# Performance work log

Hardware: AMD Instinct MI355X
Metric: run time of the kernel (lower is better)

Reference implementation:

```python
import jax, jax.numpy as jnp
import numpy as np

N_NODES = 50000
N_EDGES = 640000
N_REL = 8
D_IN = 128
D_HID = 128
D_OUT = 64


def setup_inputs() -> dict:
    key = jax.random.key(0)
    ks = jax.random.split(key, 10)
    x = jax.random.normal(ks[0], (N_NODES, D_IN), dtype=jnp.float32)
    edge_src = jax.random.randint(ks[1], (N_EDGES,), 0, N_NODES, dtype=jnp.int32)
    edge_dst = jax.random.randint(ks[2], (N_EDGES,), 0, N_NODES, dtype=jnp.int32)
    edge_type = jax.random.randint(ks[3], (N_EDGES,), 0, N_REL, dtype=jnp.int32)
    # Glorot-ish scaling for stability
    W1 = jax.random.normal(ks[4], (N_REL, D_IN, D_HID), dtype=jnp.float32) / np.sqrt(D_IN)
    root1 = jax.random.normal(ks[5], (D_IN, D_HID), dtype=jnp.float32) / np.sqrt(D_IN)
    b1 = jnp.zeros((D_HID,), dtype=jnp.float32)
    W2 = jax.random.normal(ks[6], (N_REL, D_HID, D_OUT), dtype=jnp.float32) / np.sqrt(D_HID)
    root2 = jax.random.normal(ks[7], (D_HID, D_OUT), dtype=jnp.float32) / np.sqrt(D_HID)
    b2 = jnp.zeros((D_OUT,), dtype=jnp.float32)
    return {"x": x, "edge_src": edge_src, "edge_dst": edge_dst, "edge_type": edge_type,
            "W1": W1, "root1": root1, "b1": b1, "W2": W2, "root2": root2, "b2": b2}


def rgcn_conv(x, edge_src, edge_dst, edge_type, W, W_root, b):
    """RGCNConv with default per-relation mean aggregation + root weight + bias."""
    N = x.shape[0]
    R, _, O = W.shape
    # Transform all nodes under all relation weights once: [N, R, O]
    xW = jnp.einsum('nd,rdo->nro', x, W)
    # Gather per-edge relation-specific messages: [E, O]
    msg = xW[edge_src, edge_type]
    # Segment per (dst, relation) for mean aggregation
    seg = edge_dst.astype(jnp.int32) * R + edge_type.astype(jnp.int32)
    cnt = jax.ops.segment_sum(jnp.ones_like(edge_type, dtype=x.dtype), seg, num_segments=N * R)
    agg = jax.ops.segment_sum(msg, seg, num_segments=N * R)  # [N*R, O]
    agg = agg / jnp.maximum(cnt, 1.0)[:, None]
    rel_sum = agg.reshape(N, R, O).sum(axis=1)  # [N, O]
    return rel_sum + x @ W_root + b


def reference(x, edge_src, edge_dst, edge_type, W1, root1, b1, W2, root2, b2):
    h = rgcn_conv(x, edge_src, edge_dst, edge_type, W1, root1, b1)
    h = rgcn_conv(h, edge_src, edge_dst, edge_type, W2, root2, b2)
    return jax.nn.sigmoid(h)
```

## Files before the change

### kernel.cpp

```cpp
#include <hip/hip_runtime.h>
#include <math.h>

#define NN 50000
#define NE 640000
#define NR 8
#define KT 1152
#define KA 1024
#define SCAN_N (NN * NR)
#define SCAN_CH 2048
#define SCAN_NB ((SCAN_N + SCAN_CH - 1) / SCAN_CH)

typedef __attribute__((ext_vector_type(8))) _Float16 half8;
typedef __attribute__((ext_vector_type(8))) short short8;
typedef __attribute__((ext_vector_type(4))) float f32x4;
typedef const void __attribute__((address_space(1))) gvoid_t;
typedef void __attribute__((address_space(3))) svoid_t;

__device__ __forceinline__ unsigned short f2h(float f) {
    _Float16 h = (_Float16)f;
    return __builtin_bit_cast(unsigned short, h);
}
__device__ __forceinline__ float h2f(unsigned short u) {
    return (float)__builtin_bit_cast(_Float16, u);
}

__global__ __launch_bounds__(256) void count_kernel(const int* __restrict__ dst,
                                                    const int* __restrict__ typ,
                                                    int* __restrict__ cnt, int E) {
    int e = blockIdx.x * 256 + threadIdx.x;
    if (e < E) atomicAdd(&cnt[dst[e] * NR + typ[e]], 1);
}

__global__ __launch_bounds__(256) void inv_kernel(const int* __restrict__ cnt,
                                                  float* __restrict__ inv, int n) {
    int i = blockIdx.x * 256 + threadIdx.x;
    if (i < n) {
        int c = cnt[i];
        inv[i] = 1.0f / (float)(c > 1 ? c : 1);
    }
}

__global__ __launch_bounds__(256) void scan1_kernel(const int* __restrict__ cnt,
                                                    int* __restrict__ loc,
                                                    int* __restrict__ bsum) {
    __shared__ int s[256];
    const int t = threadIdx.x;
    const int base = blockIdx.x * SCAN_CH + t * 8;
    int v[8];
    int sum = 0;
#pragma unroll
    for (int j = 0; j < 8; ++j) {
        int idx = base + j;
        v[j] = (idx < SCAN_N) ? cnt[idx] : 0;
        sum += v[j];
    }
    s[t] = sum;
    __syncthreads();
    for (int off = 1; off < 256; off <<= 1) {
        int u = (t >= off) ? s[t - off] : 0;
        __syncthreads();
        s[t] += u;
        __syncthreads();
    }
    int run = (t == 0) ? 0 : s[t - 1];
#pragma unroll
    for (int j = 0; j < 8; ++j) {
        int idx = base + j;
        if (idx < SCAN_N) loc[idx] = run;
        run += v[j];
    }
    if (t == 255) bsum[blockIdx.x] = s[255];
}

__global__ __launch_bounds__(256) void scan2_kernel(const int* __restrict__ bsum,
                                                    int* __restrict__ boff, int nb) {
    __shared__ int s[256];
    const int t = threadIdx.x;
    s[t] = (t < nb) ? bsum[t] : 0;
    __syncthreads();
    for (int off = 1; off < 256; off <<= 1) {
        int u = (t >= off) ? s[t - off] : 0;
        __syncthreads();
        s[t] += u;
        __syncthreads();
    }
    if (t < nb) boff[t] = (t == 0) ? 0 : s[t - 1];
    if (t == nb - 1) boff[nb] = s[t];
}

__global__ __launch_bounds__(256) void scan3_kernel(int* __restrict__ rowptr,
                                                    int* __restrict__ start,
                                                    const int* __restrict__ boff, int nb) {
    const int b = blockIdx.x, t = threadIdx.x;
    const int add = boff[b];
#pragma unroll
    for (int j = 0; j < 8; ++j) {
        int idx = b * SCAN_CH + t * 8 + j;
        if (idx < SCAN_N) {
            int v = rowptr[idx] + add;
            rowptr[idx] = v;
            start[idx] = v;
        }
    }
    if (b == 0 && t == 0) rowptr[SCAN_N] = boff[nb];
}

__global__ __launch_bounds__(256) void fill_kernel(const int* __restrict__ src,
                                                   const int* __restrict__ dst,
                                                   const int* __restrict__ typ,
                                                   int* __restrict__ start,
                                                   int* __restrict__ srcrel, int E) {
    int e = blockIdx.x * 256 + threadIdx.x;
    if (e >= E) return;
    int r = typ[e];
    int pos = atomicAdd(&start[dst[e] * NR + r], 1);
    srcrel[pos] = src[e] | (r << 20);
}

__global__ __launch_bounds__(256) void cvt_kernel(const float* __restrict__ x,
                                                  unsigned short* __restrict__ xh, int n4) {
    int i = blockIdx.x * 256 + threadIdx.x;
    if (i >= n4) return;
    float4 v = ((const float4*)x)[i];
    uint2 u;
    u.x = (unsigned)f2h(v.x) | ((unsigned)f2h(v.y) << 16);
    u.y = (unsigned)f2h(v.z) | ((unsigned)f2h(v.w) << 16);
    ((uint2*)xh)[i] = u;
}

__global__ __launch_bounds__(256) void pack_b_kernel(const float* __restrict__ W,
                                                     const float* __restrict__ root,
                                                     unsigned short* __restrict__ Bt, int N) {
    int i = blockIdx.x * 256 + threadIdx.x;
    if (i >= N * KT) return;
    int k = i % KT, n = i / KT;
    float v = (k < 1024) ? W[(size_t)k * N + n] : root[(size_t)(k - 1024) * N + n];
    Bt[(size_t)n * KT + k] = f2h(v);
}

__global__ __launch_bounds__(256) void agg_kernel(const int* __restrict__ rp,
                                                  const int* __restrict__ srcrel,
                                                  const float* __restrict__ inv,
                                                  const unsigned short* __restrict__ X,
                                                  unsigned short* __restrict__ A) {
    __shared__ float acc[4][NR][128];
    const int slot = threadIdx.x >> 6, lane = threadIdx.x & 63;
    const int w = blockIdx.x * 4 + slot;
    if (w >= NN) return;

#pragma unroll
    for (int r = 0; r < NR; ++r)
        *(float2*)&acc[slot][r][lane * 2] = make_float2(0.f, 0.f);

    const unsigned int* X2 = (const unsigned int*)X;
    const int beg = rp[w * NR], end = rp[w * NR + NR];

    int i = beg;
    const int n2 = beg + ((end - beg) & ~1);
    for (; i < n2; i += 2) {
        int p0 = srcrel[i], p1 = srcrel[i + 1];
        unsigned h0 = X2[(size_t)(p0 & 0xFFFFF) * 64 + lane];
        unsigned h1 = X2[(size_t)(p1 & 0xFFFFF) * 64 + lane];
        {
            float2* a = (float2*)&acc[slot][((unsigned)p0) >> 20][lane * 2];
            float2 c = *a;
            c.x += h2f((unsigned short)(h0 & 0xFFFFu));
            c.y += h2f((unsigned short)(h0 >> 16));
            *a = c;
        }
        {
            float2* a = (float2*)&acc[slot][((unsigned)p1) >> 20][lane * 2];
            float2 c = *a;
            c.x += h2f((unsigned short)(h1 & 0xFFFFu));
            c.y += h2f((unsigned short)(h1 >> 16));
            *a = c;
        }
    }
    if (i < end) {
        int p0 = srcrel[i];
        unsigned h0 = X2[(size_t)(p0 & 0xFFFFF) * 64 + lane];
        float2* a = (float2*)&acc[slot][((unsigned)p0) >> 20][lane * 2];
        float2 c = *a;
        c.x += h2f((unsigned short)(h0 & 0xFFFFu));
        c.y += h2f((unsigned short)(h0 >> 16));
        *a = c;
    }

    unsigned int* Arow = (unsigned int*)(A + (size_t)w * KA);
#pragma unroll
    for (int r = 0; r < NR; ++r) {
        float sc = inv[w * NR + r];
        float2 v = *(float2*)&acc[slot][r][lane * 2];
        Arow[r * 64 + lane] = (unsigned)f2h(v.x * sc) | ((unsigned)f2h(v.y * sc) << 16);
    }
}

template <int NT, bool FINAL>
__global__ __launch_bounds__(256) void gemm_f16(const unsigned short* __restrict__ A,
                                                const unsigned short* __restrict__ Aroot,
                                                const unsigned short* __restrict__ Bt,
                                                const float* __restrict__ bias,
                                                void* __restrict__ Cout) {
    __shared__ __align__(16) unsigned short As[64 * 64];
    __shared__ __align__(16) unsigned short Bs[NT * 64];
    const int t = threadIdx.x;
    const int w = t >> 6, lane = t & 63;
    const int q = lane >> 4, m = lane & 15;
    const int wr = w >> 1, wc = w & 1;
    const int bm = blockIdx.x * 64;
    constexpr int WNB = NT / 32;

    f32x4 acc[2][WNB];
#pragma unroll
    for (int mb = 0; mb < 2; ++mb)
#pragma unroll
        for (int nb = 0; nb < WNB; ++nb) acc[mb][nb] = (f32x4)0.f;

    const int srow = lane >> 3, schk = lane & 7;

    for (int k0 = 0; k0 < KT; k0 += 64) {
#pragma unroll
        for (int ii = 0; ii < 2; ++ii) {
            int i = w * 2 + ii;
            int grow = bm + i * 8 + srow;
            if (grow >= NN) grow = NN - 1;
            const unsigned short* g =
                (k0 < KA) ? A + (size_t)grow * KA + k0 + schk * 8
                          : Aroot + (size_t)grow * 128 + (k0 - KA) + schk * 8;
            __builtin_amdgcn_global_load_lds((gvoid_t*)g, (svoid_t*)(As + i * 512), 16, 0, 0);
        }
#pragma unroll
        for (int ii = 0; ii < NT / 32; ++ii) {
            int i = w * (NT / 32) + ii;
            int row = i * 8 + srow;
            const unsigned short* g = Bt + (size_t)row * KT + k0 + schk * 8;
            __builtin_amdgcn_global_load_lds((gvoid_t*)g, (svoid_t*)(Bs + i * 512), 16, 0, 0);
        }
        __syncthreads();
#pragma unroll
        for (int s = 0; s < 2; ++s) {
            half8 af[2], bf[WNB];
#pragma unroll
            for (int mb = 0; mb < 2; ++mb)
                af[mb] = __builtin_bit_cast(half8,
                    *(const short8*)(As + (wr * 32 + mb * 16 + m) * 64 + s * 32 + q * 8));
#pragma unroll
            for (int nb = 0; nb < WNB; ++nb)
                bf[nb] = __builtin_bit_cast(half8,
                    *(const short8*)(Bs + (wc * (NT / 2) + nb * 16 + m) * 64 + s * 32 + q * 8));
#pragma unroll
            for (int mb = 0; mb < 2; ++mb)
#pragma unroll
                for (int nb = 0; nb < WNB; ++nb)
                    acc[mb][nb] = __builtin_amdgcn_mfma_f32_16x16x32_f16(af[mb], bf[nb],
                                                                         acc[mb][nb], 0, 0, 0);
        }
        __syncthreads();
    }

#pragma unroll
    for (int mb = 0; mb < 2; ++mb)
#pragma unroll
        for (int nb = 0; nb < WNB; ++nb) {
            int col = wc * (NT / 2) + nb * 16 + m;
            float bv = bias[col];
#pragma unroll
            for (int j = 0; j < 4; ++j) {
                int grow = bm + wr * 32 + mb * 16 + q * 4 + j;
                if (grow < NN) {
                    float v = acc[mb][nb][j] + bv;
                    if (FINAL)
                        ((float*)Cout)[(size_t)grow * NT + col] = 1.f / (1.f + __expf(-v));
                    else
                        ((unsigned short*)Cout)[(size_t)grow * NT + col] = f2h(v);
                }
            }
        }
}

extern "C" void kernel_launch(void* const* d_in, const int* in_sizes, int n_in,
                              void* d_out, int out_size, void* d_ws, size_t ws_size,
                              hipStream_t stream) {
    const float* x     = (const float*)d_in[0];
    const int*   esrc  = (const int*)d_in[1];
    const int*   edst  = (const int*)d_in[2];
    const int*   etyp  = (const int*)d_in[3];
    const float* W1    = (const float*)d_in[4];
    const float* root1 = (const float*)d_in[5];
    const float* b1    = (const float*)d_in[6];
    const float* W2    = (const float*)d_in[7];
    const float* root2 = (const float*)d_in[8];
    const float* b2    = (const float*)d_in[9];
    float* out = (float*)d_out;

    char* ws = (char*)d_ws;
    unsigned short* Bt1    = (unsigned short*)ws; ws += (size_t)128 * KT * 2;
    unsigned short* Bt2    = (unsigned short*)ws; ws += (size_t)64 * KT * 2;
    int*            cnt    = (int*)ws;            ws += (size_t)SCAN_N * 4;
    float*          inv    = (float*)ws;          ws += (size_t)SCAN_N * 4;
    int*            rp     = (int*)ws;            ws += (size_t)(SCAN_N + 64) * 4;
    int*            start  = (int*)ws;            ws += (size_t)SCAN_N * 4;
    int*            bsum   = (int*)ws;            ws += (size_t)256 * 4;
    int*            boff   = (int*)ws;            ws += (size_t)257 * 4;
    int*            srcrel = (int*)ws;            ws += (size_t)NE * 4;
    unsigned short* xh     = (unsigned short*)ws; ws += (size_t)NN * 128 * 2;
    unsigned short* h1b    = (unsigned short*)ws; ws += (size_t)NN * 128 * 2;
    unsigned short* Abig   = (unsigned short*)ws;

    hipMemsetAsync(cnt, 0, (size_t)SCAN_N * 4, stream);
    count_kernel<<<(NE + 255) / 256, 256, 0, stream>>>(edst, etyp, cnt, NE);
    inv_kernel<<<(SCAN_N + 255) / 256, 256, 0, stream>>>(cnt, inv, SCAN_N);
    scan1_kernel<<<SCAN_NB, 256, 0, stream>>>(cnt, rp, bsum);
    scan2_kernel<<<1, 256, 0, stream>>>(bsum, boff, SCAN_NB);
    scan3_kernel<<<SCAN_NB, 256, 0, stream>>>(rp, start, boff, SCAN_NB);
    fill_kernel<<<(NE + 255) / 256, 256, 0, stream>>>(esrc, edst, etyp, start, srcrel, NE);

    cvt_kernel<<<(NN * 32 + 255) / 256, 256, 0, stream>>>(x, xh, NN * 32);
    pack_b_kernel<<<(128 * KT + 255) / 256, 256, 0, stream>>>(W1, root1, Bt1, 128);
    pack_b_kernel<<<(64 * KT + 255) / 256, 256, 0, stream>>>(W2, root2, Bt2, 64);

    const int agrid = (NN + 3) / 4;
    const int ggrid = (NN + 63) / 64;

    agg_kernel<<<agrid, 256, 0, stream>>>(rp, srcrel, inv, xh, Abig);
    gemm_f16<128, false><<<ggrid, 256, 0, stream>>>(Abig, xh, Bt1, b1, h1b);

    agg_kernel<<<agrid, 256, 0, stream>>>(rp, srcrel, inv, h1b, Abig);
    gemm_f16<64, true><<<ggrid, 256, 0, stream>>>(Abig, h1b, Bt2, b2, out);
}
```

Measured before the change: 348.9 us.

## Reorder RGCN to transform-then-gather and fuse mean, root and bias into aggregation

Instead of aggregating raw features per relation into a wide A matrix and running a K=1152 GEMM, each layer first computes x times all relation and root weights into an N×(9·O) fp16 buffer. An aggregation kernel then gathers relation-specific rows per edge, scales by inverse counts, and adds root and bias (plus sigmoid at the end). This removes the shared-memory per-relation accumulators and shrinks layer-2 gather width, at the cost of writing a large intermediate transform buffer.

```diff
diff --git a/kernel.cpp b/kernel.cpp
--- a/kernel.cpp
+++ b/kernel.cpp
@@ -4,8 +4,6 @@
 #define NN 50000
 #define NE 640000
 #define NR 8
-#define KT 1152
-#define KA 1024
 #define SCAN_N (NN * NR)
 #define SCAN_CH 2048
 #define SCAN_NB ((SCAN_N + SCAN_CH - 1) / SCAN_CH)
@@ -130,128 +128,70 @@
 
 __global__ __launch_bounds__(256) void pack_b_kernel(const float* __restrict__ W,
                                                      const float* __restrict__ root,
-                                                     unsigned short* __restrict__ Bt, int N) {
+                                                     unsigned short* __restrict__ Bt, int O) {
     int i = blockIdx.x * 256 + threadIdx.x;
-    if (i >= N * KT) return;
-    int k = i % KT, n = i / KT;
-    float v = (k < 1024) ? W[(size_t)k * N + n] : root[(size_t)(k - 1024) * N + n];
-    Bt[(size_t)n * KT + k] = f2h(v);
-}
-
-__global__ __launch_bounds__(256) void agg_kernel(const int* __restrict__ rp,
-                                                  const int* __restrict__ srcrel,
-                                                  const float* __restrict__ inv,
-                                                  const unsigned short* __restrict__ X,
-                                                  unsigned short* __restrict__ A) {
-    __shared__ float acc[4][NR][128];
-    const int slot = threadIdx.x >> 6, lane = threadIdx.x & 63;
-    const int w = blockIdx.x * 4 + slot;
-    if (w >= NN) return;
-
-#pragma unroll
-    for (int r = 0; r < NR; ++r)
-        *(float2*)&acc[slot][r][lane * 2] = make_float2(0.f, 0.f);
-
-    const unsigned int* X2 = (const unsigned int*)X;
-    const int beg = rp[w * NR], end = rp[w * NR + NR];
-
-    int i = beg;
-    const int n2 = beg + ((end - beg) & ~1);
-    for (; i < n2; i += 2) {
-        int p0 = srcrel[i], p1 = srcrel[i + 1];
-        unsigned h0 = X2[(size_t)(p0 & 0xFFFFF) * 64 + lane];
-        unsigned h1 = X2[(size_t)(p1 & 0xFFFFF) * 64 + lane];
-        {
-            float2* a = (float2*)&acc[slot][((unsigned)p0) >> 20][lane * 2];
-            float2 c = *a;
-            c.x += h2f((unsigned short)(h0 & 0xFFFFu));
-            c.y += h2f((unsigned short)(h0 >> 16));
-            *a = c;
-        }
-        {
-            float2* a = (float2*)&acc[slot][((unsigned)p1) >> 20][lane * 2];
-            float2 c = *a;
-            c.x += h2f((unsigned short)(h1 & 0xFFFFu));
-            c.y += h2f((unsigned short)(h1 >> 16));
-            *a = c;
-        }
-    }
-    if (i < end) {
-        int p0 = srcrel[i];
-        unsigned h0 = X2[(size_t)(p0 & 0xFFFFF) * 64 + lane];
-        float2* a = (float2*)&acc[slot][((unsigned)p0) >> 20][lane * 2];
-        float2 c = *a;
-        c.x += h2f((unsigned short)(h0 & 0xFFFFu));
-        c.y += h2f((unsigned short)(h0 >> 16));
-        *a = c;
-    }
-
-    unsigned int* Arow = (unsigned int*)(A + (size_t)w * KA);
-#pragma unroll
-    for (int r = 0; r < NR; ++r) {
-        float sc = inv[w * NR + r];
-        float2 v = *(float2*)&acc[slot][r][lane * 2];
-        Arow[r * 64 + lane] = (unsigned)f2h(v.x * sc) | ((unsigned)f2h(v.y * sc) << 16);
-    }
-}
-
-template <int NT, bool FINAL>
-__global__ __launch_bounds__(256) void gemm_f16(const unsigned short* __restrict__ A,
-                                                const unsigned short* __restrict__ Aroot,
-                                                const unsigned short* __restrict__ Bt,
-                                                const float* __restrict__ bias,
-                                                void* __restrict__ Cout) {
+    int NTOT = 9 * O;
+    if (i >= NTOT * 128) return;
+    int k = i & 127, n = i >> 7;
+    float v = (n < 8 * O) ? W[(size_t)(n / O) * 128 * O + (size_t)k * O + (n % O)]
+                          : root[(size_t)k * O + (n - 8 * O)];
+    Bt[(size_t)n * 128 + k] = f2h(v);
+}
+
+template <int LDC>
+__global__ __launch_bounds__(256) void gemm_xw(const unsigned short* __restrict__ A,
+                                               const unsigned short* __restrict__ Bt,
+                                               unsigned short* __restrict__ C) {
     __shared__ __align__(16) unsigned short As[64 * 64];
-    __shared__ __align__(16) unsigned short Bs[NT * 64];
+    __shared__ __align__(16) unsigned short Bs[64 * 64];
     const int t = threadIdx.x;
     const int w = t >> 6, lane = t & 63;
     const int q = lane >> 4, m = lane & 15;
     const int wr = w >> 1, wc = w & 1;
-    const int bm = blockIdx.x * 64;
-    constexpr int WNB = NT / 32;
-
-    f32x4 acc[2][WNB];
+    const int bm = blockIdx.y * 64;
+    const int bn = blockIdx.x * 64;
+
+    f32x4 acc[2][2];
 #pragma unroll
     for (int mb = 0; mb < 2; ++mb)
 #pragma unroll
-        for (int nb = 0; nb < WNB; ++nb) acc[mb][nb] = (f32x4)0.f;
+        for (int nb = 0; nb < 2; ++nb) acc[mb][nb] = (f32x4)0.f;
 
     const int srow = lane >> 3, schk = lane & 7;
 
-    for (int k0 = 0; k0 < KT; k0 += 64) {
+#pragma unroll
+    for (int kc = 0; kc < 2; ++kc) {
+        const int k0 = kc * 64;
 #pragma unroll
         for (int ii = 0; ii < 2; ++ii) {
             int i = w * 2 + ii;
             int grow = bm + i * 8 + srow;
             if (grow >= NN) grow = NN - 1;
-            const unsigned short* g =
-                (k0 < KA) ? A + (size_t)grow * KA + k0 + schk * 8
-                          : Aroot + (size_t)grow * 128 + (k0 - KA) + schk * 8;
+            const unsigned short* g = A + (size_t)grow * 128 + k0 + schk * 8;
             __builtin_amdgcn_global_load_lds((gvoid_t*)g, (svoid_t*)(As + i * 512), 16, 0, 0);
         }
 #pragma unroll
-        for (int ii = 0; ii < NT / 32; ++ii) {
-            int i = w * (NT / 32) + ii;
-            int row = i * 8 + srow;
-            const unsigned short* g = Bt + (size_t)row * KT + k0 + schk * 8;
+        for (int ii = 0; ii < 2; ++ii) {
+            int i = w * 2 + ii;
+            const unsigned short* g = Bt + (size_t)(bn + i * 8 + srow) * 128 + k0 + schk * 8;
             __builtin_amdgcn_global_load_lds((gvoid_t*)g, (svoid_t*)(Bs + i * 512), 16, 0, 0);
         }
         __syncthreads();
 #pragma unroll
         for (int s = 0; s < 2; ++s) {
-            half8 af[2], bf[WNB];
+            half8 af[2], bf[2];
 #pragma unroll
             for (int mb = 0; mb < 2; ++mb)
                 af[mb] = __builtin_bit_cast(half8,
                     *(const short8*)(As + (wr * 32 + mb * 16 + m) * 64 + s * 32 + q * 8));
 #pragma unroll
-            for (int nb = 0; nb < WNB; ++nb)
+            for (int nb = 0; nb < 2; ++nb)
                 bf[nb] = __builtin_bit_cast(half8,
-                    *(const short8*)(Bs + (wc * (NT / 2) + nb * 16 + m) * 64 + s * 32 + q * 8));
+                    *(const short8*)(Bs + (wc * 32 + nb * 16 + m) * 64 + s * 32 + q * 8));
 #pragma unroll
             for (int mb = 0; mb < 2; ++mb)
 #pragma unroll
-                for (int nb = 0; nb < WNB; ++nb)
+                for (int nb = 0; nb < 2; ++nb)
                     acc[mb][nb] = __builtin_amdgcn_mfma_f32_16x16x32_f16(af[mb], bf[nb],
                                                                          acc[mb][nb], 0, 0, 0);
         }
@@ -261,21 +201,92 @@
 #pragma unroll
     for (int mb = 0; mb < 2; ++mb)
 #pragma unroll
-        for (int nb = 0; nb < WNB; ++nb) {
-            int col = wc * (NT / 2) + nb * 16 + m;
-            float bv = bias[col];
+        for (int nb = 0; nb < 2; ++nb) {
+            int col = bn + wc * 32 + nb * 16 + m;
 #pragma unroll
             for (int j = 0; j < 4; ++j) {
                 int grow = bm + wr * 32 + mb * 16 + q * 4 + j;
-                if (grow < NN) {
-                    float v = acc[mb][nb][j] + bv;
-                    if (FINAL)
-                        ((float*)Cout)[(size_t)grow * NT + col] = 1.f / (1.f + __expf(-v));
-                    else
-                        ((unsigned short*)Cout)[(size_t)grow * NT + col] = f2h(v);
-                }
+                if (grow < NN)
+                    C[(size_t)grow * LDC + col] = f2h(acc[mb][nb][j]);
             }
         }
+}
+
+template <int O, bool FINAL>
+__global__ __launch_bounds__(256) void agg_kernel(const int* __restrict__ rp,
+                                                  const int* __restrict__ srcrel,
+                                                  const float* __restrict__ inv,
+                                                  const unsigned short* __restrict__ XW,
+                                                  const float* __restrict__ bias,
+                                                  void* __restrict__ Hout) {
+    __shared__ float sinv[4][8];
+    const int slot = threadIdx.x >> 6, lane = threadIdx.x & 63;
+    const int w = blockIdx.x * 4 + slot;
+    if (w >= NN) return;
+    if (lane < 8) sinv[slot][lane] = inv[w * NR + lane];
+
+    const int beg = rp[w * NR], end = rp[w * NR + NR];
+    constexpr int LDC2 = 9 * O / 2;
+
+    if (O == 128) {
+        const unsigned int* X2 = (const unsigned int*)XW;
+        float2 acc = make_float2(0.f, 0.f);
+        int i = beg;
+        for (; i + 3 < end; i += 4) {
+            int p0 = srcrel[i], p1 = srcrel[i + 1], p2 = srcrel[i + 2], p3 = srcrel[i + 3];
+            unsigned g0 = X2[(size_t)(p0 & 0xFFFFF) * LDC2 + (((unsigned)p0) >> 20) * 64 + lane];
+            unsigned g1 = X2[(size_t)(p1 & 0xFFFFF) * LDC2 + (((unsigned)p1) >> 20) * 64 + lane];
+            unsigned g2 = X2[(size_t)(p2 & 0xFFFFF) * LDC2 + (((unsigned)p2) >> 20) * 64 + lane];
+            unsigned g3 = X2[(size_t)(p3 & 0xFFFFF) * LDC2 + (((unsigned)p3) >> 20) * 64 + lane];
+            float s0 = sinv[slot][((unsigned)p0) >> 20];
+            float s1 = sinv[slot][((unsigned)p1) >> 20];
+            float s2 = sinv[slot][((unsigned)p2) >> 20];
+            float s3 = sinv[slot][((unsigned)p3) >> 20];
+            acc.x += h2f((unsigned short)(g0 & 0xFFFFu)) * s0;
+            acc.y += h2f((unsigned short)(g0 >> 16)) * s0;
+            acc.x += h2f((unsigned short)(g1 & 0xFFFFu)) * s1;
+            acc.y += h2f((unsigned short)(g1 >> 16)) * s1;
+            acc.x += h2f((unsigned short)(g2 & 0xFFFFu)) * s2;
+            acc.y += h2f((unsigned short)(g2 >> 16)) * s2;
+            acc.x += h2f((unsigned short)(g3 & 0xFFFFu)) * s3;
+            acc.y += h2f((unsigned short)(g3 >> 16)) * s3;
+        }
+        for (; i < end; ++i) {
+            int p0 = srcrel[i];
+            unsigned g0 = X2[(size_t)(p0 & 0xFFFFF) * LDC2 + (((unsigned)p0) >> 20) * 64 + lane];
+            float s0 = sinv[slot][((unsigned)p0) >> 20];
+            acc.x += h2f((unsigned short)(g0 & 0xFFFFu)) * s0;
+            acc.y += h2f((unsigned short)(g0 >> 16)) * s0;
+        }
+        unsigned rt = X2[(size_t)w * LDC2 + 512 + lane];
+        float2 bv = ((const float2*)bias)[lane];
+        float vx = acc.x + h2f((unsigned short)(rt & 0xFFFFu)) + bv.x;
+        float vy = acc.y + h2f((unsigned short)(rt >> 16)) + bv.y;
+        ((unsigned int*)Hout)[(size_t)w * 64 + lane] =
+            (unsigned)f2h(vx) | ((unsigned)f2h(vy) << 16);
+    } else {
+        constexpr int LDC = 9 * O;
+        float acc = 0.f;
+        int i = beg;
+        for (; i + 3 < end; i += 4) {
+            int p0 = srcrel[i], p1 = srcrel[i + 1], p2 = srcrel[i + 2], p3 = srcrel[i + 3];
+            unsigned short g0 = XW[(size_t)(p0 & 0xFFFFF) * LDC + (((unsigned)p0) >> 20) * 64 + lane];
+            unsigned short g1 = XW[(size_t)(p1 & 0xFFFFF) * LDC + (((unsigned)p1) >> 20) * 64 + lane];
+            unsigned short g2 = XW[(size_t)(p2 & 0xFFFFF) * LDC + (((unsigned)p2) >> 20) * 64 + lane];
+            unsigned short g3 = XW[(size_t)(p3 & 0xFFFFF) * LDC + (((unsigned)p3) >> 20) * 64 + lane];
+            acc += h2f(g0) * sinv[slot][((unsigned)p0) >> 20];
+            acc += h2f(g1) * sinv[slot][((unsigned)p1) >> 20];
+            acc += h2f(g2) * sinv[slot][((unsigned)p2) >> 20];
+            acc += h2f(g3) * sinv[slot][((unsigned)p3) >> 20];
+        }
+        for (; i < end; ++i) {
+            int p0 = srcrel[i];
+            unsigned short g0 = XW[(size_t)(p0 & 0xFFFFF) * LDC + (((unsigned)p0) >> 20) * 64 + lane];
+            acc += h2f(g0) * sinv[slot][((unsigned)p0) >> 20];
+        }
+        float v = acc + h2f(XW[(size_t)w * LDC + 512 + lane]) + bias[lane];
+        ((float*)Hout)[(size_t)w * 64 + lane] = 1.f / (1.f + __expf(-v));
+    }
 }
 
 extern "C" void kernel_launch(void* const* d_in, const int* in_sizes, int n_in,
@@ -294,8 +305,8 @@
     float* out = (float*)d_out;
 
     char* ws = (char*)d_ws;
-    unsigned short* Bt1    = (unsigned short*)ws; ws += (size_t)128 * KT * 2;
-    unsigned short* Bt2    = (unsigned short*)ws; ws += (size_t)64 * KT * 2;
+    unsigned short* Bt1    = (unsigned short*)ws; ws += (size_t)1152 * 128 * 2;
+    unsigned short* Bt2    = (unsigned short*)ws; ws += (size_t)576 * 128 * 2;
     int*            cnt    = (int*)ws;            ws += (size_t)SCAN_N * 4;
     float*          inv    = (float*)ws;          ws += (size_t)SCAN_N * 4;
     int*            rp     = (int*)ws;            ws += (size_t)(SCAN_N + 64) * 4;
@@ -305,7 +316,8 @@
     int*            srcrel = (int*)ws;            ws += (size_t)NE * 4;
     unsigned short* xh     = (unsigned short*)ws; ws += (size_t)NN * 128 * 2;
     unsigned short* h1b    = (unsigned short*)ws; ws += (size_t)NN * 128 * 2;
-    unsigned short* Abig   = (unsigned short*)ws;
+    unsigned short* xW     = (unsigned short*)ws;
+    unsigned short* xW2    = xW;
 
     hipMemsetAsync(cnt, 0, (size_t)SCAN_N * 4, stream);
     count_kernel<<<(NE + 255) / 256, 256, 0, stream>>>(edst, etyp, cnt, NE);
@@ -316,15 +328,15 @@
     fill_kernel<<<(NE + 255) / 256, 256, 0, stream>>>(esrc, edst, etyp, start, srcrel, NE);
 
     cvt_kernel<<<(NN * 32 + 255) / 256, 256, 0, stream>>>(x, xh, NN * 32);
-    pack_b_kernel<<<(128 * KT + 255) / 256, 256, 0, stream>>>(W1, root1, Bt1, 128);
-    pack_b_kernel<<<(64 * KT + 255) / 256, 256, 0, stream>>>(W2, root2, Bt2, 64);
+    pack_b_kernel<<<(1152 * 128 + 255) / 256, 256, 0, stream>>>(W1, root1, Bt1, 128);
+    pack_b_kernel<<<(576 * 128 + 255) / 256, 256, 0, stream>>>(W2, root2, Bt2, 64);
 
     const int agrid = (NN + 3) / 4;
-    const int ggrid = (NN + 63) / 64;
-
-    agg_kernel<<<agrid, 256, 0, stream>>>(rp, srcrel, inv, xh, Abig);
-    gemm_f16<128, false><<<ggrid, 256, 0, stream>>>(Abig, xh, Bt1, b1, h1b);
-
-    agg_kernel<<<agrid, 256, 0, stream>>>(rp, srcrel, inv, h1b, Abig);
-    gemm_f16<64, true><<<ggrid, 256, 0, stream>>>(Abig, h1b, Bt2, b2, out);
-}
+    const int gy = (NN + 63) / 64;
+
+    gemm_xw<1152><<<dim3(1152 / 64, gy), 256, 0, stream>>>(xh, Bt1, xW);
+    agg_kernel<128, false><<<agrid, 256, 0, stream>>>(rp, srcrel, inv, xW, b1, h1b);
+
+    gemm_xw<576><<<dim3(576 / 64, gy), 256, 0, stream>>>(h1b, Bt2, xW2);
+    agg_kernel<64, true><<<agrid, 256, 0, stream>>>(rp, srcrel, inv, xW2, b2, out);
+}
```

Measured after the change: 330.0 us. -5.4%, faster.
